# Kernel tuning notes

Hardware: AMD Instinct MI355X
Metric: run time of the kernel (lower is better)

The kernel has to match this reference:

```python
import jax, jax.numpy as jnp
import numpy as np

B, S, HID, H = 2, 2048, 1024, 16
D = HID // H
LAMBDA_INIT = 0.8
GN_EPS = 1e-5


def setup_inputs() -> dict:
    rng = jax.random.key(0)
    ks = jax.random.split(rng, 12)
    w = 0.02
    return {
        "query": jax.random.normal(ks[0], (B, S, HID), dtype=jnp.float32),
        "key": jax.random.normal(ks[1], (B, S, HID), dtype=jnp.float32),
        "value": jax.random.normal(ks[2], (B, S, HID), dtype=jnp.float32),
        "attention_mask": jnp.ones((B, S), dtype=jnp.float32),
        # params ([in, out] layout; x @ W)
        "Wq": jax.random.normal(ks[3], (HID, H * D * 2), dtype=jnp.float32) * w,
        "Wk": jax.random.normal(ks[4], (HID, H * D * 2), dtype=jnp.float32) * w,
        "Wv": jax.random.normal(ks[5], (HID, H * D), dtype=jnp.float32) * w,
        "Wo": jax.random.normal(ks[6], (H * D, HID), dtype=jnp.float32) * w,
        "lam_q1": jax.random.normal(ks[7], (D,), dtype=jnp.float32),
        "lam_q2": jax.random.normal(ks[8], (D,), dtype=jnp.float32),
        "lam_k1": jax.random.normal(ks[9], (D,), dtype=jnp.float32),
        "lam_k2": jax.random.normal(ks[10], (D,), dtype=jnp.float32),
        "gn_weight": jnp.ones((H * D,), dtype=jnp.float32),
        "gn_bias": jnp.zeros((H * D,), dtype=jnp.float32),
    }


def reference(query, key, value, attention_mask, Wq, Wk, Wv, Wo,
              lam_q1, lam_q2, lam_k1, lam_k2, gn_weight, gn_bias):
    b, s, hid = query.shape
    h, d = H, hid // H
    rs = 1.0 / jnp.sqrt(jnp.asarray(d, query.dtype))

    q = (query @ Wq).reshape(b, s, h, 2 * d).transpose(0, 2, 1, 3)   # [b,h,s,2d]
    k = (key @ Wk).reshape(b, s, h, 2 * d).transpose(0, 2, 1, 3)
    v = (value @ Wv).reshape(b, s, h, d).transpose(0, 2, 1, 3)       # [b,h,s,d]

    Q1, Q2 = q[..., :d], q[..., d:]
    K1, K2 = k[..., :d], k[..., d:]
    s1 = jnp.einsum('bhqd,bhkd->bhqk', Q1, K1) * rs
    s2 = jnp.einsum('bhqd,bhkd->bhqk', Q2, K2) * rs

    # ALiBi bias: slopes[h] * (pos_q - pos_k), subtracted from scores
    pos = jnp.arange(s, dtype=query.dtype)
    slopes = 2.0 ** (-8.0 * jnp.arange(1, h + 1, dtype=query.dtype) / h)
    alibi = slopes[None, :, None, None] * (pos[:, None] - pos[None, :])[None, None]
    causal = jnp.triu(jnp.full((s, s), -1e9, dtype=query.dtype), k=1)[None, None]
    pad = (1.0 - attention_mask)[:, None, None, :] * -1e9
    add = -alibi + causal + pad

    w1 = jax.nn.softmax(s1 + add, axis=-1)
    w2 = jax.nn.softmax(s2 + add, axis=-1)

    lam = (jnp.exp(jnp.dot(lam_q1, lam_k1))
           - jnp.exp(jnp.dot(lam_q2, lam_k2)) + LAMBDA_INIT)
    dw = w1 - lam * w2

    attn = jnp.einsum('bhqk,bhkd->bhqd', dw, v).transpose(0, 2, 1, 3)  # [b,s,h,d]

    # GroupNorm(groups=h, channels=h*d) over [b, C, L]: per (b, head) normalize over (seq, d)
    mean = attn.mean(axis=(1, 3), keepdims=True)
    var = ((attn - mean) ** 2).mean(axis=(1, 3), keepdims=True)
    normed = (attn - mean) / jnp.sqrt(var + GN_EPS)
    normed = normed * gn_weight.reshape(1, 1, h, d) + gn_bias.reshape(1, 1, h, d)

    out = normed * (1.0 - LAMBDA_INIT)
    return out.reshape(b, s, h * d) @ Wo
```

## Files before the change

kernel.cpp:

```cpp
#include <hip/hip_runtime.h>
#include <cstdint>
#include <cstddef>

#define SQ 2048
#define NH 16
#define DH 64
#define HIDN 1024

typedef __attribute__((ext_vector_type(8))) short bf16x8;
typedef __attribute__((ext_vector_type(4))) float f32x4;
typedef __attribute__((ext_vector_type(2))) unsigned u32x2;

__device__ inline short f2b(float x) {
  union { float f; unsigned u; } un; un.f = x;
  unsigned r = un.u + 0x7fffu + ((un.u >> 16) & 1u);
  return (short)(r >> 16);
}

__device__ inline unsigned cvt_pk(float lo, float hi) {
  unsigned r;
  asm("v_cvt_pk_bf16_f32 %0, %1, %2" : "=v"(r) : "v"(lo), "v"(hi));
  return r;
}

__device__ inline f32x4 mfma16(u32x2 a, u32x2 b, f32x4 c) {
  asm("v_mfma_f32_16x16x16_bf16 %0, %1, %2, %0" : "+v"(c) : "v"(a), "v"(b));
  return c;
}

__device__ inline void gl_lds16(const void* g, void* l) {
  __builtin_amdgcn_global_load_lds(
      (const __attribute__((address_space(1))) void*)g,
      (__attribute__((address_space(3))) void*)l, 16, 0, 0);
}

__global__ __launch_bounds__(256) void qkv_to_bf16(const float4* __restrict__ q,
                                                   const float4* __restrict__ k,
                                                   const float4* __restrict__ v,
                                                   short4* __restrict__ out) {
  int i = blockIdx.x * 256 + threadIdx.x;
  const float4* src = (i < 1048576) ? q : ((i < 2097152) ? k : v);
  float4 val = src[i & 1048575];
  short4 o;
  o.x = f2b(val.x); o.y = f2b(val.y); o.z = f2b(val.z); o.w = f2b(val.w);
  out[i] = o;
}

__global__ __launch_bounds__(256) void wconv4(const float* __restrict__ Wq,
                                              const float* __restrict__ Wk,
                                              const float* __restrict__ Wv,
                                              const float* __restrict__ Wo,
                                              short* __restrict__ WqT, short* __restrict__ WkT,
                                              short* __restrict__ WvT, short* __restrict__ WoT) {
  __shared__ float t[32][33];
  int z = blockIdx.z;
  int N = (z < 2) ? 2048 : 1024;
  if (blockIdx.x * 32 >= N) return;
  const float* W = (z == 0) ? Wq : (z == 1) ? Wk : (z == 2) ? Wv : Wo;
  short* Wt = (z == 0) ? WqT : (z == 1) ? WkT : (z == 2) ? WvT : WoT;
  const int K = 1024;
  int n0 = blockIdx.x * 32, k0 = blockIdx.y * 32;
  int tx = threadIdx.x & 31, ty = threadIdx.x >> 5;
#pragma unroll
  for (int r = 0; r < 4; ++r)
    t[ty + r * 8][tx] = W[(size_t)(k0 + ty + r * 8) * N + n0 + tx];
  __syncthreads();
#pragma unroll
  for (int r = 0; r < 4; ++r)
    Wt[(size_t)(n0 + ty + r * 8) * K + k0 + tx] = f2b(t[tx][ty + r * 8]);
}

__global__ void lam_k(const float* __restrict__ q1, const float* __restrict__ q2,
                      const float* __restrict__ k1, const float* __restrict__ k2,
                      float* __restrict__ out) {
  int i = threadIdx.x;
  float d1 = q1[i] * k1[i], d2 = q2[i] * k2[i];
#pragma unroll
  for (int x = 1; x < 64; x <<= 1) { d1 += __shfl_xor(d1, x); d2 += __shfl_xor(d2, x); }
  if (i == 0) out[0] = __expf(d1) - __expf(d2) + 0.8f;
}

__global__ __launch_bounds__(256) void padk(const float* __restrict__ mask,
                                            float* __restrict__ padl2) {
  int i = blockIdx.x * 256 + threadIdx.x;
  padl2[i] = (1.0f - mask[i]) * (-1.0e9f) * 1.44269504089f;
}

#define STAGEP(buf, k0s)                                                        \
  {                                                                             \
    _Pragma("unroll") for (int it_ = 0; it_ < 4; ++it_) {                       \
      int idx_ = it_ * 256 + tid;                                               \
      int row_ = idx_ >> 3, u_ = idx_ & 7;                                      \
      int us_ = (u_ ^ (row_ & 7)) << 3;                                         \
      gl_lds16(Ag + (size_t)row_ * 1024 + (k0s) + us_, &As[buf][idx_ << 3]);    \
      gl_lds16(Bg + (size_t)row_ * 1024 + (k0s) + us_, &Bs[buf][idx_ << 3]);    \
    }                                                                           \
  }

__global__ __launch_bounds__(256) void proj3(const short* __restrict__ Abase,
                                             const short* __restrict__ Btbase,
                                             short* __restrict__ QKout,
                                             short* __restrict__ Vtb) {
  __shared__ __align__(16) short As[2][128 * 64];
  __shared__ __align__(16) short Bs[2][128 * 64];
  const int bid = blockIdx.x;
  const int wk = (bid & 7) * 160 + (bid >> 3);
  int z, my, nx;
  if (wk < 1024) { z = wk >> 9; int r = wk & 511; my = r >> 4; nx = r & 15; }
  else { z = 2; int r = wk - 1024; my = r >> 3; nx = r & 7; }

  const int tid = threadIdx.x;
  const int lane = tid & 63, w = tid >> 6;
  const int l15 = lane & 15, lhi = lane >> 4;
  const int sw7 = l15 & 7;
  const int u0 = (lhi ^ sw7) << 3, u1 = ((4 + lhi) ^ sw7) << 3;
  const int wr = w >> 1, wc = w & 1;
  const int m0 = my * 128, n0 = nx * 128;

  const short* Ag = Abase + (size_t)z * 4194304 + (size_t)m0 * 1024;
  const short* Bg = Btbase + (size_t)z * 2097152 + (size_t)n0 * 1024;

  f32x4 acc[4][4];
#pragma unroll
  for (int i = 0; i < 4; ++i)
#pragma unroll
    for (int j = 0; j < 4; ++j) acc[i][j] = (f32x4){0.f, 0.f, 0.f, 0.f};

  int cur = 0;
  STAGEP(0, 0);
  asm volatile("s_waitcnt vmcnt(0)" ::: "memory");
  __builtin_amdgcn_s_barrier();

  for (int kt = 0; kt < 16; ++kt) {
    if (kt < 15) STAGEP(cur ^ 1, (kt + 1) * 64);
#pragma unroll
    for (int kh = 0; kh < 2; ++kh) {
      const int uk = kh ? u1 : u0;
      bf16x8 af[4], bfr[4];
#pragma unroll
      for (int mi = 0; mi < 4; ++mi)
        af[mi] = *(const bf16x8*)&As[cur][((wr * 64 + mi * 16 + l15) << 6) + uk];
#pragma unroll
      for (int ni = 0; ni < 4; ++ni)
        bfr[ni] = *(const bf16x8*)&Bs[cur][((wc * 64 + ni * 16 + l15) << 6) + uk];
#pragma unroll
      for (int mi = 0; mi < 4; ++mi)
#pragma unroll
        for (int ni = 0; ni < 4; ++ni)
          acc[mi][ni] = __builtin_amdgcn_mfma_f32_16x16x32_bf16(af[mi], bfr[ni], acc[mi][ni], 0, 0, 0);
    }
    asm volatile("s_waitcnt vmcnt(0)" ::: "memory");
    __builtin_amdgcn_s_barrier();
    cur ^= 1;
  }

#pragma unroll
  for (int mi = 0; mi < 4; ++mi) {
#pragma unroll
    for (int ni = 0; ni < 4; ++ni) {
#pragma unroll
      for (int j = 0; j < 4; ++j) {
        int m = m0 + wr * 64 + mi * 16 + (lhi << 2) + j;
        int n = n0 + wc * 64 + ni * 16 + l15;
        float v = acc[mi][ni][j];
        int s = m & (SQ - 1), bb = m >> 11;
        if (z < 2) {
          int h = n >> 7, t = n & 127, path = t >> 6, tt = t & 63;
          (QKout + (size_t)z * 8388608)
              [((((size_t)(bb * NH + h) * 2 + path) * SQ + s) << 6) + tt] = f2b(v);
        } else {
          int h = n >> 6, t = n & 63;
          Vtb[(((size_t)(bb * NH + h) << 6) + t) * SQ + s] = f2b(v);
        }
      }
    }
  }
}

__global__ __launch_bounds__(256) void gemm_out(const short* __restrict__ A,
                                                const short* __restrict__ Bt,
                                                float* __restrict__ Cout) {
  __shared__ __align__(16) short As[2][128 * 64];
  __shared__ __align__(16) short Bs[2][128 * 64];
  const int bid = blockIdx.x;
  const int wk = (bid & 7) * 32 + (bid >> 3);
  const int my = wk >> 3, nx = wk & 7;

  const int tid = threadIdx.x;
  const int lane = tid & 63, w = tid >> 6;
  const int l15 = lane & 15, lhi = lane >> 4;
  const int sw7 = l15 & 7;
  const int u0 = (lhi ^ sw7) << 3, u1 = ((4 + lhi) ^ sw7) << 3;
  const int wr = w >> 1, wc = w & 1;
  const int m0 = my * 128, n0 = nx * 128;

  const short* Ag = A + (size_t)m0 * 1024;
  const short* Bg = Bt + (size_t)n0 * 1024;

  f32x4 acc[4][4];
#pragma unroll
  for (int i = 0; i < 4; ++i)
#pragma unroll
    for (int j = 0; j < 4; ++j) acc[i][j] = (f32x4){0.f, 0.f, 0.f, 0.f};

  int cur = 0;
  STAGEP(0, 0);
  asm volatile("s_waitcnt vmcnt(0)" ::: "memory");
  __builtin_amdgcn_s_barrier();

  for (int kt = 0; kt < 16; ++kt) {
    if (kt < 15) STAGEP(cur ^ 1, (kt + 1) * 64);
#pragma unroll
    for (int kh = 0; kh < 2; ++kh) {
      const int uk = kh ? u1 : u0;
      bf16x8 af[4], bfr[4];
#pragma unroll
      for (int mi = 0; mi < 4; ++mi)
        af[mi] = *(const bf16x8*)&As[cur][((wr * 64 + mi * 16 + l15) << 6) + uk];
#pragma unroll
      for (int ni = 0; ni < 4; ++ni)
        bfr[ni] = *(const bf16x8*)&Bs[cur][((wc * 64 + ni * 16 + l15) << 6) + uk];
#pragma unroll
      for (int mi = 0; mi < 4; ++mi)
#pragma unroll
        for (int ni = 0; ni < 4; ++ni)
          acc[mi][ni] = __builtin_amdgcn_mfma_f32_16x16x32_bf16(af[mi], bfr[ni], acc[mi][ni], 0, 0, 0);
    }
    asm volatile("s_waitcnt vmcnt(0)" ::: "memory");
    __builtin_amdgcn_s_barrier();
    cur ^= 1;
  }

#pragma unroll
  for (int mi = 0; mi < 4; ++mi)
#pragma unroll
    for (int ni = 0; ni < 4; ++ni)
#pragma unroll
      for (int j = 0; j < 4; ++j) {
        int m = m0 + wr * 64 + mi * 16 + (lhi << 2) + j;
        int n = n0 + wc * 64 + ni * 16 + l15;
        Cout[(size_t)m * 1024 + n] = acc[mi][ni][j];
      }
}

__global__ __launch_bounds__(256) void diff_attn(
    const short* __restrict__ Qp, const short* __restrict__ Kp,
    const short* __restrict__ Vt, const float* __restrict__ padl2,
    const float* __restrict__ lamp, float* __restrict__ attn,
    float* __restrict__ part) {
  __shared__ __align__(16) short K1s[2][64 * 64];
  __shared__ __align__(16) short K2s[2][64 * 64];
  __shared__ __align__(16) short Vts[2][64 * 64];
  __shared__ float red[8];

  const int bid = blockIdx.x;
  const int rk = bid >> 5, bh = bid & 31;
  const int qtA = 31 - rk, qtB = rk;
  const int ntA = qtA + 1, ntT = ntA + qtB + 1;
  const int b = bh >> 4, h = bh & 15;
  const int tid = threadIdx.x, lane = tid & 63, w = tid >> 6;
  const int l15 = lane & 15, lhi = lane >> 4;
  const int sw7 = l15 & 7;
  const int u0 = (lhi ^ sw7) << 3, u1 = ((4 + lhi) ^ sw7) << 3;

  const float L2E = 1.44269504089f;
  const float slope = exp2f(-0.5f * (float)(h + 1));
  const float SC = 0.125f * L2E;
  const float sl2 = slope * L2E;

  f32x4 ck[4];
#pragma unroll
  for (int cf = 0; cf < 4; ++cf)
#pragma unroll
    for (int j = 0; j < 4; ++j)
      ck[cf][j] = sl2 * (float)(16 * cf + 4 * lhi + j);

  const short* Q1g = Qp + (((size_t)bh * 2 + 0) * SQ) * DH;
  const short* Q2g = Qp + (((size_t)bh * 2 + 1) * SQ) * DH;
  const short* K1g = Kp + (((size_t)bh * 2 + 0) * SQ) * DH;
  const short* K2g = Kp + (((size_t)bh * 2 + 1) * SQ) * DH;
  const short* Vtg = Vt + (size_t)bh * DH * SQ;
  const float* padb = padl2 + (b << 11);

  int ucf[4];
#pragma unroll
  for (int cf = 0; cf < 4; ++cf)
    ucf[cf] = (((2 * cf + (lhi >> 1)) ^ sw7) << 1) + (lhi & 1);

  const int sidx0 = tid, sidx1 = 256 + tid;
  const int srow0 = sidx0 >> 3, sus0 = ((sidx0 & 7) ^ (srow0 & 7)) << 3;
  const int srow1 = sidx1 >> 3, sus1 = ((sidx1 & 7) ^ (srow1 & 7)) << 3;

#define STAGE(buf, k0s)                                                          \
  {                                                                              \
    gl_lds16(K1g + (size_t)((k0s) + srow0) * DH + sus0, &K1s[buf][sidx0 << 3]);  \
    gl_lds16(K2g + (size_t)((k0s) + srow0) * DH + sus0, &K2s[buf][sidx0 << 3]);  \
    gl_lds16(Vtg + (size_t)srow0 * SQ + (k0s) + sus0, &Vts[buf][sidx0 << 3]);    \
    gl_lds16(K1g + (size_t)((k0s) + srow1) * DH + sus1, &K1s[buf][sidx1 << 3]);  \
    gl_lds16(K2g + (size_t)((k0s) + srow1) * DH + sus1, &K2s[buf][sidx1 << 3]);  \
    gl_lds16(Vtg + (size_t)srow1 * SQ + (k0s) + sus1, &Vts[buf][sidx1 << 3]);    \
  }

  int cur = 0;
  int itg = 0;
  STAGE(0, 0);
  asm volatile("s_waitcnt vmcnt(0)" ::: "memory");
  __builtin_amdgcn_s_barrier();

  const float lamv = lamp[0];

  for (int ph = 0; ph < 2; ++ph) {
    const int qt = ph ? qtB : qtA;
    const int nt = qt + 1;
    const int wq0 = qt * 64 + (w << 4);
    const int q = wq0 + l15;
    const float qb8 = sl2 * (float)q + 8.0f;

    bf16x8 aq[2][2];
#pragma unroll
    for (int kk = 0; kk < 2; ++kk) {
      aq[0][kk] = *(const bf16x8*)&Q1g[(size_t)q * DH + kk * 32 + lhi * 8];
      aq[1][kk] = *(const bf16x8*)&Q2g[(size_t)q * DH + kk * 32 + lhi * 8];
    }
    f32x4 cq[4];
#pragma unroll
    for (int cf = 0; cf < 4; ++cf)
#pragma unroll
      for (int j = 0; j < 4; ++j) cq[cf][j] = ck[cf][j] - qb8;

    f32x4 acc[2][4];
    float ll[2] = {0.f, 0.f};
#pragma unroll
    for (int p = 0; p < 2; ++p)
#pragma unroll
      for (int i = 0; i < 4; ++i) acc[p][i] = (f32x4){0.f, 0.f, 0.f, 0.f};

    for (int kt = 0; kt < nt; ++kt, ++itg) {
      const int k0 = kt << 6;
      int g = itg + 1;
      if (g < ntT) {
        int k0n = ((g < ntA) ? g : g - ntA) << 6;
        STAGE(cur ^ 1, k0n);
      }

      const float t0 = sl2 * (float)k0;
      f32x4 base4[4];
#pragma unroll
      for (int cf = 0; cf < 4; ++cf) {
        f32x4 p4 = *(const f32x4*)&padb[k0 + 16 * cf + 4 * lhi];
#pragma unroll
        for (int j = 0; j < 4; ++j) base4[cf][j] = cq[cf][j] + (t0 + p4[j]);
      }
      const bool diag = (kt == nt - 1);

      u32x2 pa[2][4];
#pragma unroll
      for (int p = 0; p < 2; ++p) {
        const short* Ks = (p == 0) ? K1s[cur] : K2s[cur];
        f32x4 sv[4];
#pragma unroll
        for (int cf = 0; cf < 4; ++cf) {
          int rb = (cf * 16 + l15) << 6;
          f32x4 z = (f32x4){0.f, 0.f, 0.f, 0.f};
          bf16x8 ka = *(const bf16x8*)&Ks[rb + u0];
          bf16x8 kb = *(const bf16x8*)&Ks[rb + u1];
          sv[cf] = __builtin_amdgcn_mfma_f32_16x16x32_bf16(ka, aq[p][0], z, 0, 0, 0);
          sv[cf] = __builtin_amdgcn_mfma_f32_16x16x32_bf16(kb, aq[p][1], sv[cf], 0, 0, 0);
        }
        float rsum = 0.f;
#pragma unroll
        for (int cf = 0; cf < 4; ++cf) {
          float pv[4];
#pragma unroll
          for (int j = 0; j < 4; ++j) pv[j] = sv[cf][j] * SC + base4[cf][j];
          if (diag) {
#pragma unroll
            for (int j = 0; j < 4; ++j) {
              int kc = k0 + 16 * cf + 4 * lhi + j;
              pv[j] = (kc > q) ? -1.0e9f : pv[j];
            }
          }
          float e0 = exp2f(pv[0]);
          float e1 = exp2f(pv[1]);
          float e2 = exp2f(pv[2]);
          float e3 = exp2f(pv[3]);
          rsum += (e0 + e1) + (e2 + e3);
          pa[p][cf][0] = cvt_pk(e0, e1);
          pa[p][cf][1] = cvt_pk(e2, e3);
        }
        ll[p] += rsum;
      }

#pragma unroll
      for (int df = 0; df < 4; ++df) {
        const u32x2* vrow = (const u32x2*)&Vts[cur][(df * 16 + l15) << 6];
#pragma unroll
        for (int cf = 0; cf < 4; ++cf) {
          u32x2 vb = vrow[ucf[cf]];
          acc[0][df] = mfma16(pa[0][cf], vb, acc[0][df]);
          acc[1][df] = mfma16(pa[1][cf], vb, acc[1][df]);
        }
      }

      asm volatile("s_waitcnt vmcnt(0)" ::: "memory");
      __builtin_amdgcn_s_barrier();
      cur ^= 1;
    }

#pragma unroll
    for (int p = 0; p < 2; ++p) {
      ll[p] += __shfl_xor(ll[p], 16);
      ll[p] += __shfl_xor(ll[p], 32);
    }
    float li1 = 1.0f / ll[0], li2 = lamv / ll[1];
    float li1b[4], li2b[4];
#pragma unroll
    for (int j = 0; j < 4; ++j) {
      li1b[j] = __shfl(li1, (lhi << 2) + j);
      li2b[j] = __shfl(li2, (lhi << 2) + j);
    }
    float lsum = 0.f, lsq = 0.f;
#pragma unroll
    for (int df = 0; df < 4; ++df)
#pragma unroll
      for (int j = 0; j < 4; ++j) {
        int qq = wq0 + (lhi << 2) + j;
        float o = acc[0][df][j] * li1b[j] - acc[1][df][j] * li2b[j];
        attn[((size_t)b * SQ + qq) * HIDN + (h << 6) + (df << 4) + l15] = o;
        lsum += o; lsq += o * o;
      }
#pragma unroll
    for (int x = 1; x < 64; x <<= 1) {
      lsum += __shfl_xor(lsum, x);
      lsq += __shfl_xor(lsq, x);
    }
    if (lane == 0) { red[w] = lsum; red[4 + w] = lsq; }
    __syncthreads();
    if (tid == 0) {
      part[((size_t)bh * 32 + qt) * 2] = red[0] + red[1] + red[2] + red[3];
      part[((size_t)bh * 32 + qt) * 2 + 1] = red[4] + red[5] + red[6] + red[7];
    }
  }
#undef STAGE
}

__global__ void stats_fin(const float* __restrict__ part, float* __restrict__ mi) {
  int bh = threadIdx.x;
  float s = 0.f, ss = 0.f;
  for (int t = 0; t < 32; ++t) {
    s += part[(bh * 32 + t) * 2];
    ss += part[(bh * 32 + t) * 2 + 1];
  }
  float n = (float)(SQ * DH);
  float mean = s / n;
  float var = ss / n - mean * mean;
  mi[bh * 2] = mean;
  mi[bh * 2 + 1] = rsqrtf(var + 1e-5f);
}

__global__ __launch_bounds__(256) void gn_apply(const float* __restrict__ attn,
                                                const float* __restrict__ mi,
                                                const float* __restrict__ gnw,
                                                const float* __restrict__ gnb,
                                                short* __restrict__ X) {
  size_t i = (size_t)blockIdx.x * 256 + threadIdx.x;
  size_t base = i << 2;
  int r = (int)(base >> 10);
  int c = (int)(base & 1023);
  int bh = ((r >> 11) << 4) + (c >> 6);
  float mean = mi[bh * 2], inv = mi[bh * 2 + 1];
  float4 a = *(const float4*)&attn[base];
  short4 o;
  o.x = f2b(((a.x - mean) * inv * gnw[c + 0] + gnb[c + 0]) * 0.2f);
  o.y = f2b(((a.y - mean) * inv * gnw[c + 1] + gnb[c + 1]) * 0.2f);
  o.z = f2b(((a.z - mean) * inv * gnw[c + 2] + gnb[c + 2]) * 0.2f);
  o.w = f2b(((a.w - mean) * inv * gnw[c + 3] + gnb[c + 3]) * 0.2f);
  *(short4*)&X[base] = o;
}

extern "C" void kernel_launch(void* const* d_in, const int* in_sizes, int n_in,
                              void* d_out, int out_size, void* d_ws, size_t ws_size,
                              hipStream_t stream) {
  const float* query = (const float*)d_in[0];
  const float* key = (const float*)d_in[1];
  const float* value = (const float*)d_in[2];
  const float* mask = (const float*)d_in[3];
  const float* Wq = (const float*)d_in[4];
  const float* Wk = (const float*)d_in[5];
  const float* Wv = (const float*)d_in[6];
  const float* Wo = (const float*)d_in[7];
  const float* lq1 = (const float*)d_in[8];
  const float* lq2 = (const float*)d_in[9];
  const float* lk1 = (const float*)d_in[10];
  const float* lk2 = (const float*)d_in[11];
  const float* gnw = (const float*)d_in[12];
  const float* gnb = (const float*)d_in[13];

  char* ws = (char*)d_ws;
  short* WqT = (short*)(ws + 0);
  short* WkT = (short*)(ws + 4194304);
  short* WvT = (short*)(ws + 8388608);
  short* WoT = (short*)(ws + 10485760);
  short* qb = (short*)(ws + 12582912);
  short* Qp = (short*)(ws + 37748736);
  short* Kp = (short*)(ws + 54525952);
  short* Vtb = (short*)(ws + 71303168);
  float* attn = (float*)(ws + 12582912);
  short* X = (short*)(ws + 29360128);
  float* part = (float*)(ws + 79691776);
  float* mi = (float*)(ws + 79708160);
  float* lam = (float*)(ws + 79708416);
  float* padl2 = (float*)(ws + 79708672);

  qkv_to_bf16<<<12288, 256, 0, stream>>>((const float4*)query, (const float4*)key,
                                         (const float4*)value, (short4*)qb);
  wconv4<<<dim3(64, 32, 4), 256, 0, stream>>>(Wq, Wk, Wv, Wo, WqT, WkT, WvT, WoT);
  lam_k<<<1, 64, 0, stream>>>(lq1, lq2, lk1, lk2, lam);
  padk<<<16, 256, 0, stream>>>(mask, padl2);

  proj3<<<dim3(1280), 256, 0, stream>>>(qb, WqT, Qp, Vtb);

  diff_attn<<<dim3(512), 256, 0, stream>>>(Qp, Kp, Vtb, padl2, lam, attn, part);
  stats_fin<<<1, 32, 0, stream>>>(part, mi);
  gn_apply<<<4096, 256, 0, stream>>>(attn, mi, gnw, gnb, X);
  gemm_out<<<dim3(256), 256, 0, stream>>>(X, WoT, (float*)d_out);
}
```

Measured before the change: 221.5 us.

## Split GEMM K-tiles into half-stages with finer waitcnt and MFMA priority

Both bf16 GEMMs (the QKV projection and the output projection) now stage each 64-wide K tile as two 32-wide halves in separate LDS buffers. Global-to-LDS loads for the next tile are issued right after the fragment reads, and `vmcnt(4)` leaves the newest half-stage in flight instead of draining all loads. MFMA blocks run under raised wave priority. The XOR LDS swizzle is dropped for the narrower row layout, which may bring back bank conflicts. Separately, stats_fin reduces the per-head partials with 1024 threads and lane shuffles instead of 32 serial loops.

```diff
diff --git a/kernel.cpp b/kernel.cpp
--- a/kernel.cpp
+++ b/kernel.cpp
@@ -86,23 +86,20 @@
   padl2[i] = (1.0f - mask[i]) * (-1.0e9f) * 1.44269504089f;
 }
 
-#define STAGEP(buf, k0s)                                                        \
-  {                                                                             \
-    _Pragma("unroll") for (int it_ = 0; it_ < 4; ++it_) {                       \
-      int idx_ = it_ * 256 + tid;                                               \
-      int row_ = idx_ >> 3, u_ = idx_ & 7;                                      \
-      int us_ = (u_ ^ (row_ & 7)) << 3;                                         \
-      gl_lds16(Ag + (size_t)row_ * 1024 + (k0s) + us_, &As[buf][idx_ << 3]);    \
-      gl_lds16(Bg + (size_t)row_ * 1024 + (k0s) + us_, &Bs[buf][idx_ << 3]);    \
-    }                                                                           \
+#define STG(dst, srcp, kt, kk)                                                        \
+  {                                                                                   \
+    gl_lds16(srcp + (size_t)r0_ * 1024 + ((kt) << 6) + ((kk) << 5) + c0_,             \
+             &dst[ch0_ << 3]);                                                        \
+    gl_lds16(srcp + (size_t)r1_ * 1024 + ((kt) << 6) + ((kk) << 5) + c1_,             \
+             &dst[ch1_ << 3]);                                                        \
   }
 
 __global__ __launch_bounds__(256) void proj3(const short* __restrict__ Abase,
                                              const short* __restrict__ Btbase,
                                              short* __restrict__ QKout,
                                              short* __restrict__ Vtb) {
-  __shared__ __align__(16) short As[2][128 * 64];
-  __shared__ __align__(16) short Bs[2][128 * 64];
+  __shared__ __align__(16) short As[2][2][128 * 32];
+  __shared__ __align__(16) short Bs[2][2][128 * 32];
   const int bid = blockIdx.x;
   const int wk = (bid & 7) * 160 + (bid >> 3);
   int z, my, nx;
@@ -112,46 +109,56 @@
   const int tid = threadIdx.x;
   const int lane = tid & 63, w = tid >> 6;
   const int l15 = lane & 15, lhi = lane >> 4;
-  const int sw7 = l15 & 7;
-  const int u0 = (lhi ^ sw7) << 3, u1 = ((4 + lhi) ^ sw7) << 3;
   const int wr = w >> 1, wc = w & 1;
   const int m0 = my * 128, n0 = nx * 128;
 
   const short* Ag = Abase + (size_t)z * 4194304 + (size_t)m0 * 1024;
   const short* Bg = Btbase + (size_t)z * 2097152 + (size_t)n0 * 1024;
 
+  const int ch0_ = tid, ch1_ = tid + 256;
+  const int r0_ = ch0_ >> 2, c0_ = (ch0_ & 3) << 3;
+  const int r1_ = ch1_ >> 2, c1_ = (ch1_ & 3) << 3;
+
   f32x4 acc[4][4];
 #pragma unroll
   for (int i = 0; i < 4; ++i)
 #pragma unroll
     for (int j = 0; j < 4; ++j) acc[i][j] = (f32x4){0.f, 0.f, 0.f, 0.f};
 
-  int cur = 0;
-  STAGEP(0, 0);
-  asm volatile("s_waitcnt vmcnt(0)" ::: "memory");
+  STG(As[0][0], Ag, 0, 0); STG(Bs[0][0], Bg, 0, 0);
+  STG(As[0][1], Ag, 0, 1); STG(Bs[0][1], Bg, 0, 1);
+  asm volatile("s_waitcnt vmcnt(4)" ::: "memory");
   __builtin_amdgcn_s_barrier();
 
   for (int kt = 0; kt < 16; ++kt) {
-    if (kt < 15) STAGEP(cur ^ 1, (kt + 1) * 64);
-#pragma unroll
-    for (int kh = 0; kh < 2; ++kh) {
-      const int uk = kh ? u1 : u0;
+    const int buf = kt & 1;
+#pragma unroll
+    for (int kk = 0; kk < 2; ++kk) {
+      const short* Ah = As[buf][kk];
+      const short* Bh = Bs[buf][kk];
       bf16x8 af[4], bfr[4];
 #pragma unroll
       for (int mi = 0; mi < 4; ++mi)
-        af[mi] = *(const bf16x8*)&As[cur][((wr * 64 + mi * 16 + l15) << 6) + uk];
+        af[mi] = *(const bf16x8*)&Ah[((wr * 64 + mi * 16 + l15) << 5) + (lhi << 3)];
 #pragma unroll
       for (int ni = 0; ni < 4; ++ni)
-        bfr[ni] = *(const bf16x8*)&Bs[cur][((wc * 64 + ni * 16 + l15) << 6) + uk];
+        bfr[ni] = *(const bf16x8*)&Bh[((wc * 64 + ni * 16 + l15) << 5) + (lhi << 3)];
+      if (kt < 15) {
+        STG(As[buf ^ 1][kk], Ag, kt + 1, kk);
+        STG(Bs[buf ^ 1][kk], Bg, kt + 1, kk);
+      }
+      __builtin_amdgcn_s_barrier();
+      __builtin_amdgcn_s_setprio(1);
 #pragma unroll
       for (int mi = 0; mi < 4; ++mi)
 #pragma unroll
         for (int ni = 0; ni < 4; ++ni)
           acc[mi][ni] = __builtin_amdgcn_mfma_f32_16x16x32_bf16(af[mi], bfr[ni], acc[mi][ni], 0, 0, 0);
-    }
-    asm volatile("s_waitcnt vmcnt(0)" ::: "memory");
-    __builtin_amdgcn_s_barrier();
-    cur ^= 1;
+      __builtin_amdgcn_s_setprio(0);
+      if (kt < 15) asm volatile("s_waitcnt vmcnt(4)" ::: "memory");
+      else         asm volatile("s_waitcnt vmcnt(0)" ::: "memory");
+      __builtin_amdgcn_s_barrier();
+    }
   }
 
 #pragma unroll
@@ -180,8 +187,8 @@
 __global__ __launch_bounds__(256) void gemm_out(const short* __restrict__ A,
                                                 const short* __restrict__ Bt,
                                                 float* __restrict__ Cout) {
-  __shared__ __align__(16) short As[2][128 * 64];
-  __shared__ __align__(16) short Bs[2][128 * 64];
+  __shared__ __align__(16) short As[2][2][128 * 32];
+  __shared__ __align__(16) short Bs[2][2][128 * 32];
   const int bid = blockIdx.x;
   const int wk = (bid & 7) * 32 + (bid >> 3);
   const int my = wk >> 3, nx = wk & 7;
@@ -189,46 +196,56 @@
   const int tid = threadIdx.x;
   const int lane = tid & 63, w = tid >> 6;
   const int l15 = lane & 15, lhi = lane >> 4;
-  const int sw7 = l15 & 7;
-  const int u0 = (lhi ^ sw7) << 3, u1 = ((4 + lhi) ^ sw7) << 3;
   const int wr = w >> 1, wc = w & 1;
   const int m0 = my * 128, n0 = nx * 128;
 
   const short* Ag = A + (size_t)m0 * 1024;
   const short* Bg = Bt + (size_t)n0 * 1024;
 
+  const int ch0_ = tid, ch1_ = tid + 256;
+  const int r0_ = ch0_ >> 2, c0_ = (ch0_ & 3) << 3;
+  const int r1_ = ch1_ >> 2, c1_ = (ch1_ & 3) << 3;
+
   f32x4 acc[4][4];
 #pragma unroll
   for (int i = 0; i < 4; ++i)
 #pragma unroll
     for (int j = 0; j < 4; ++j) acc[i][j] = (f32x4){0.f, 0.f, 0.f, 0.f};
 
-  int cur = 0;
-  STAGEP(0, 0);
-  asm volatile("s_waitcnt vmcnt(0)" ::: "memory");
+  STG(As[0][0], Ag, 0, 0); STG(Bs[0][0], Bg, 0, 0);
+  STG(As[0][1], Ag, 0, 1); STG(Bs[0][1], Bg, 0, 1);
+  asm volatile("s_waitcnt vmcnt(4)" ::: "memory");
   __builtin_amdgcn_s_barrier();
 
   for (int kt = 0; kt < 16; ++kt) {
-    if (kt < 15) STAGEP(cur ^ 1, (kt + 1) * 64);
-#pragma unroll
-    for (int kh = 0; kh < 2; ++kh) {
-      const int uk = kh ? u1 : u0;
+    const int buf = kt & 1;
+#pragma unroll
+    for (int kk = 0; kk < 2; ++kk) {
+      const short* Ah = As[buf][kk];
+      const short* Bh = Bs[buf][kk];
       bf16x8 af[4], bfr[4];
 #pragma unroll
       for (int mi = 0; mi < 4; ++mi)
-        af[mi] = *(const bf16x8*)&As[cur][((wr * 64 + mi * 16 + l15) << 6) + uk];
+        af[mi] = *(const bf16x8*)&Ah[((wr * 64 + mi * 16 + l15) << 5) + (lhi << 3)];
 #pragma unroll
       for (int ni = 0; ni < 4; ++ni)
-        bfr[ni] = *(const bf16x8*)&Bs[cur][((wc * 64 + ni * 16 + l15) << 6) + uk];
+        bfr[ni] = *(const bf16x8*)&Bh[((wc * 64 + ni * 16 + l15) << 5) + (lhi << 3)];
+      if (kt < 15) {
+        STG(As[buf ^ 1][kk], Ag, kt + 1, kk);
+        STG(Bs[buf ^ 1][kk], Bg, kt + 1, kk);
+      }
+      __builtin_amdgcn_s_barrier();
+      __builtin_amdgcn_s_setprio(1);
 #pragma unroll
       for (int mi = 0; mi < 4; ++mi)
 #pragma unroll
         for (int ni = 0; ni < 4; ++ni)
           acc[mi][ni] = __builtin_amdgcn_mfma_f32_16x16x32_bf16(af[mi], bfr[ni], acc[mi][ni], 0, 0, 0);
-    }
-    asm volatile("s_waitcnt vmcnt(0)" ::: "memory");
-    __builtin_amdgcn_s_barrier();
-    cur ^= 1;
+      __builtin_amdgcn_s_setprio(0);
+      if (kt < 15) asm volatile("s_waitcnt vmcnt(4)" ::: "memory");
+      else         asm volatile("s_waitcnt vmcnt(0)" ::: "memory");
+      __builtin_amdgcn_s_barrier();
+    }
   }
 
 #pragma unroll
@@ -445,17 +462,19 @@
 }
 
 __global__ void stats_fin(const float* __restrict__ part, float* __restrict__ mi) {
-  int bh = threadIdx.x;
-  float s = 0.f, ss = 0.f;
-  for (int t = 0; t < 32; ++t) {
-    s += part[(bh * 32 + t) * 2];
-    ss += part[(bh * 32 + t) * 2 + 1];
-  }
-  float n = (float)(SQ * DH);
-  float mean = s / n;
-  float var = ss / n - mean * mean;
-  mi[bh * 2] = mean;
-  mi[bh * 2 + 1] = rsqrtf(var + 1e-5f);
+  int t = threadIdx.x;
+  int bh = t >> 5, i = t & 31;
+  float s = part[(bh * 32 + i) * 2];
+  float ss = part[(bh * 32 + i) * 2 + 1];
+#pragma unroll
+  for (int x = 1; x < 32; x <<= 1) { s += __shfl_xor(s, x); ss += __shfl_xor(ss, x); }
+  if (i == 0) {
+    float n = (float)(SQ * DH);
+    float mean = s / n;
+    float var = ss / n - mean * mean;
+    mi[bh * 2] = mean;
+    mi[bh * 2 + 1] = rsqrtf(var + 1e-5f);
+  }
 }
 
 __global__ __launch_bounds__(256) void gn_apply(const float* __restrict__ attn,
@@ -521,7 +540,7 @@
   proj3<<<dim3(1280), 256, 0, stream>>>(qb, WqT, Qp, Vtb);
 
   diff_attn<<<dim3(512), 256, 0, stream>>>(Qp, Kp, Vtb, padl2, lam, attn, part);
-  stats_fin<<<1, 32, 0, stream>>>(part, mi);
+  stats_fin<<<1, 1024, 0, stream>>>(part, mi);
   gn_apply<<<4096, 256, 0, stream>>>(attn, mi, gnw, gnb, X);
   gemm_out<<<dim3(256), 256, 0, stream>>>(X, WoT, (float*)d_out);
 }
```

Measured after the change: 206.7 us, median of 2. 1.07x faster.
